# Kernel optimization log

Measured on AMD Instinct MI355X. Metric: run time of the kernel, lower is better.

## Reference

```python
import jax, jax.numpy as jnp
import numpy as np

B, T, C, H = 1, 4096, 768, 12
D = C // H  # 64


def setup_inputs() -> dict:
    key = jax.random.key(0)
    k1, k2, k3, k4, k5 = jax.random.split(key, 5)
    x = jax.random.normal(k1, (B, T, C), dtype=jnp.float32)
    # causal mask: 1.0 where attention is DISALLOWED (strict upper triangle)
    mask = (1.0 - jnp.tril(jnp.ones((T, T), dtype=jnp.float32)))[None, None, :, :]
    s_attn = 1.0 / np.sqrt(C)
    W_qkv = jax.random.normal(k2, (C, 3 * C), dtype=jnp.float32) * s_attn
    b_qkv = jnp.zeros((3 * C,), dtype=jnp.float32)
    W_proj = jax.random.normal(k3, (C, C), dtype=jnp.float32) * s_attn
    b_proj = jnp.zeros((C,), dtype=jnp.float32)
    return {"x": x, "mask": mask, "W_qkv": W_qkv, "b_qkv": b_qkv,
            "W_proj": W_proj, "b_proj": b_proj}


def reference(x, mask, W_qkv, b_qkv, W_proj, b_proj):
    qkv = jnp.einsum('btc,cf->btf', x, W_qkv) + b_qkv        # [B,T,3C]
    q, k, v = jnp.split(qkv, 3, axis=2)
    # [B,T,C] -> [B,H,T,D]
    q = q.reshape(B, T, H, D).transpose(0, 2, 1, 3)
    k = k.reshape(B, T, H, D).transpose(0, 2, 1, 3)
    v = v.reshape(B, T, H, D).transpose(0, 2, 1, 3)
    att = jnp.einsum('bhqd,bhkd->bhqk', q, k) * (1.0 / jnp.sqrt(jnp.float32(D)))
    att = att + mask * (-1e9)
    att = jax.nn.softmax(att, axis=-1)                        # [B,H,T,T]
    y = jnp.einsum('bhqk,bhkd->bhqd', att, v)                 # [B,H,T,D]
    y = y.transpose(0, 2, 1, 3).reshape(B, T, C)
    return jnp.einsum('btc,cf->btf', y, W_proj) + b_proj
```

## Files before the change

kernel.cpp:

```cpp
#include <hip/hip_runtime.h>

typedef unsigned short u16t;
typedef short bf16x8 __attribute__((ext_vector_type(8)));
typedef short bf16x4 __attribute__((ext_vector_type(4)));
typedef float f32x4 __attribute__((ext_vector_type(4)));

#define T_SEQ 4096
#define NH    12
#define HD    64
#define C3    2304
#define CDIM  768
#define STRIP_KV 512
#define SLOTS 144

__device__ __forceinline__ float bf2f(u16t u) {
  union { unsigned int i; float f; } c; c.i = ((unsigned int)u) << 16; return c.f;
}
__device__ __forceinline__ u16t f2bf(float f) {
  union { float f; unsigned int i; } c; c.f = f;
  unsigned int u = c.i;
  u += 0x7fffu + ((u >> 16) & 1u);
  return (u16t)(u >> 16);
}
__device__ __forceinline__ void gload16(const u16t* g, u16t* l) {
  __builtin_amdgcn_global_load_lds((const __attribute__((address_space(1))) void*)g,
                                   (__attribute__((address_space(3))) void*)l,
                                   16, 0, 0);
}

#define BARRIER_LGKM() __asm__ __volatile__("s_waitcnt lgkmcnt(0)\n\ts_barrier" ::: "memory")

__global__ __launch_bounds__(256) void convert_to_bf16(const float* __restrict__ in,
                                                       u16t* __restrict__ out, int n) {
  int i = blockIdx.x * 256 + threadIdx.x;
  const int stride = gridDim.x * 256;
  for (; i < n; i += stride) out[i] = f2bf(in[i]);
}

__global__ __launch_bounds__(256) void transpose_weights(const float* __restrict__ Wqkv,
                                                         const float* __restrict__ Wproj,
                                                         u16t* __restrict__ WqkvT,
                                                         u16t* __restrict__ WprojT) {
  __shared__ u16t tile[32][33];
  const int z = blockIdx.z;
  const int Cc = z ? CDIM : C3;
  if (z && blockIdx.x >= (unsigned)(CDIM / 32)) return;
  const float* in = z ? Wproj : Wqkv;
  u16t* out = z ? WprojT : WqkvT;
  const int tx = threadIdx.x, ty = threadIdx.y;
  const int c0 = blockIdx.x * 32, r0 = blockIdx.y * 32;
#pragma unroll
  for (int i = 0; i < 32; i += 8)
    tile[ty + i][tx] = f2bf(in[(size_t)(r0 + ty + i) * Cc + c0 + tx]);
  __syncthreads();
#pragma unroll
  for (int i = 0; i < 32; i += 8)
    out[(size_t)(c0 + ty + i) * CDIM + r0 + tx] = tile[tx][ty + i];
}

template <int MT, int NF, bool OUTF32>
__global__ __launch_bounds__(256) void gemm_bt_bias(
    const u16t* __restrict__ A, const u16t* __restrict__ Bt,
    const float* __restrict__ bias, void* __restrict__ Cout,
    int M, int N, int K) {
  constexpr int BN = 32 * NF;
  constexpr int MI = MT / 32;
  __shared__ u16t lA[MT * 32];
  __shared__ u16t lB[BN * 32];
  const int t = threadIdx.x;
  const int lane = t & 63;
  const int wid  = t >> 6;
  const int quad = lane >> 4, l16 = lane & 15;
  const int m0 = blockIdx.y * MT, n0 = blockIdx.x * BN;
  const int wm = (wid >> 1) * (16 * MI), wn = (wid & 1) * (16 * NF);

  f32x4 acc[MI][NF];
#pragma unroll
  for (int i = 0; i < MI; ++i)
#pragma unroll
    for (int j = 0; j < NF; ++j) acc[i][j] = (f32x4){0.f, 0.f, 0.f, 0.f};

  for (int k0 = 0; k0 < K; k0 += 32) {
    {
#pragma unroll
      for (int rd = 0; rd < MT / 64; ++rd) {
        const int e = rd * 256 + t;
        gload16(A + (size_t)(m0 + (e >> 2)) * K + k0 + (e & 3) * 8, &lA[e * 8]);
      }
#pragma unroll
      for (int rd = 0; rd < NF / 2; ++rd) {
        const int e = rd * 256 + t;
        gload16(Bt + (size_t)(n0 + (e >> 2)) * K + k0 + (e & 3) * 8, &lB[e * 8]);
      }
    }
    __syncthreads();
    bf16x8 af[MI], bfr[NF];
#pragma unroll
    for (int i = 0; i < MI; ++i)
      af[i] = *(const bf16x8*)&lA[(wm + i * 16 + l16) * 32 + quad * 8];
#pragma unroll
    for (int i = 0; i < NF; ++i)
      bfr[i] = *(const bf16x8*)&lB[(wn + i * 16 + l16) * 32 + quad * 8];
#pragma unroll
    for (int i = 0; i < MI; ++i)
#pragma unroll
      for (int j = 0; j < NF; ++j)
        acc[i][j] = __builtin_amdgcn_mfma_f32_16x16x32_bf16(af[i], bfr[j], acc[i][j], 0, 0, 0);
    __syncthreads();
  }

#pragma unroll
  for (int j = 0; j < NF; ++j) {
    const int col = n0 + wn + j * 16 + l16;
    const float bv = bias[col];
#pragma unroll
    for (int i = 0; i < MI; ++i) {
      const int rowb = m0 + wm + i * 16 + quad * 4;
#pragma unroll
      for (int r = 0; r < 4; ++r) {
        const float val = acc[i][j][r] + bv;
        const size_t idx = (size_t)(rowb + r) * N + col;
        if (OUTF32) ((float*)Cout)[idx] = val;
        else        ((u16t*)Cout)[idx] = f2bf(val);
      }
    }
  }
}

#define KSTR 88
#define VSTR 80

__global__ __launch_bounds__(256, 3) void attn_partial(const u16t* __restrict__ qkv,
                                                       u16t* __restrict__ pO,
                                                       float* __restrict__ pL) {
  const int h     = blockIdx.x;
  const int strip = blockIdx.y;
  const int qt    = 31 - (int)blockIdx.z;
  const int q0 = qt * 128;
  const int kv_begin = strip * STRIP_KV;
  const int kv_end   = q0 + 128;
  if (kv_begin >= kv_end) return;
  const int kv_stop = (kv_begin + STRIP_KV < kv_end) ? kv_begin + STRIP_KV : kv_end;
  const int a = qt >> 2, b = qt & 3;
  const int slot = (a + 1) * (2 * a + b) + strip;

  __shared__ u16t lK[64 * KSTR];
  __shared__ u16t lVt[64 * VSTR];

  const int t = threadIdx.x;
  const int lane = t & 63;
  const int wid  = t >> 6;
  const int quad = lane >> 4, l16 = lane & 15;
  const int wr = q0 + wid * 32;

  const int krow = t >> 3, kcol = (t & 7) * 8;
  const int vk0 = 4 * (t >> 4);
  const int vd0 = 4 * (t & 15);
  const int vswz = (t & 3) << 3;
  const u16t* Kbase = qkv + CDIM + h * HD;
  const u16t* Vbase = qkv + 2 * CDIM + h * HD;

  bf16x8 qf[2][2];
#pragma unroll
  for (int qn = 0; qn < 2; ++qn) {
    const int row = wr + qn * 16 + l16;
#pragma unroll
    for (int kd = 0; kd < 2; ++kd)
      qf[qn][kd] = *(const bf16x8*)(qkv + (size_t)row * C3 + h * HD + kd * 32 + quad * 8);
  }

  f32x4 oaccT[4][2];
  float lacc[2] = {0.f, 0.f};
#pragma unroll
  for (int dn = 0; dn < 4; ++dn)
#pragma unroll
    for (int qn = 0; qn < 2; ++qn) oaccT[dn][qn] = (f32x4){0.f, 0.f, 0.f, 0.f};

  const float SC = 0.125f * 1.4426950408889634f;
  const int pswz = ((l16 >> 2) & 3) << 3;

  uint4 kreg0, kreg1;
  union { uint2 u; u16t hw[4]; } vreg[4];

#define LOAD_TILE(KV0)                                                        \
  do {                                                                        \
    kreg0 = *(const uint4*)(Kbase + (size_t)((KV0) + krow) * C3 + kcol);      \
    kreg1 = *(const uint4*)(Kbase + (size_t)((KV0) + krow + 32) * C3 + kcol); \
    _Pragma("unroll")                                                         \
    for (int i = 0; i < 4; ++i)                                               \
      vreg[i].u = *(const uint2*)(Vbase + (size_t)((KV0) + vk0 + i) * C3 + vd0); \
  } while (0)

#define STORE_TILE()                                                          \
  do {                                                                        \
    *(uint4*)&lK[krow * KSTR + kcol] = kreg0;                                 \
    *(uint4*)&lK[(krow + 32) * KSTR + kcol] = kreg1;                          \
    _Pragma("unroll")                                                         \
    for (int j = 0; j < 4; ++j) {                                             \
      union { uint2 u; u16t hw[4]; } w;                                       \
      w.hw[0] = vreg[0].hw[j]; w.hw[1] = vreg[1].hw[j];                       \
      w.hw[2] = vreg[2].hw[j]; w.hw[3] = vreg[3].hw[j];                       \
      *(uint2*)&lVt[(vd0 + j) * VSTR + (vk0 ^ vswz)] = w.u;                   \
    }                                                                         \
  } while (0)

  LOAD_TILE(kv_begin);
  STORE_TILE();

  for (int kv0 = kv_begin; kv0 < kv_stop; kv0 += 64) {
    const bool havenext = (kv0 + 64 < kv_stop);
    if (havenext) LOAD_TILE(kv0 + 64);
    BARRIER_LGKM();

    if (kv0 <= wr + 31) {
      f32x4 sacc[4][2];
#pragma unroll
      for (int kvt = 0; kvt < 4; ++kvt) {
        bf16x8 kf0 = *(const bf16x8*)&lK[(kvt * 16 + l16) * KSTR + quad * 8];
        bf16x8 kf1 = *(const bf16x8*)&lK[(kvt * 16 + l16) * KSTR + 32 + quad * 8];
#pragma unroll
        for (int qn = 0; qn < 2; ++qn) {
          f32x4 s = (f32x4){0.f, 0.f, 0.f, 0.f};
          s = __builtin_amdgcn_mfma_f32_16x16x32_bf16(kf0, qf[qn][0], s, 0, 0, 0);
          s = __builtin_amdgcn_mfma_f32_16x16x32_bf16(kf1, qf[qn][1], s, 0, 0, 0);
          sacc[kvt][qn] = s;
        }
      }
      const bool need_mask = (kv0 + 63 > wr);
      bf16x4 pbf[4][2];
#pragma unroll
      for (int kvt = 0; kvt < 4; ++kvt)
#pragma unroll
        for (int qn = 0; qn < 2; ++qn) {
          const int qg = wr + qn * 16 + l16;
          bf16x4 pb;
#pragma unroll
          for (int r = 0; r < 4; ++r) {
            const int kvg = kv0 + kvt * 16 + quad * 4 + r;
            float pv = __builtin_amdgcn_exp2f(sacc[kvt][qn][r] * SC);
            if (need_mask && (kvg > qg)) pv = 0.f;
            lacc[qn] += pv;
            pb[r] = (short)f2bf(pv);
          }
          pbf[kvt][qn] = pb;
        }
#pragma unroll
      for (int kvt = 0; kvt < 4; ++kvt) {
        const int kvcol = (kvt * 16 + quad * 4) ^ pswz;
#pragma unroll
        for (int dn = 0; dn < 4; ++dn) {
          bf16x4 vf = *(const bf16x4*)&lVt[(dn * 16 + l16) * VSTR + kvcol];
#pragma unroll
          for (int qn = 0; qn < 2; ++qn)
            oaccT[dn][qn] = __builtin_amdgcn_mfma_f32_16x16x16bf16_1k(
                vf, pbf[kvt][qn], oaccT[dn][qn], 0, 0, 0);
        }
      }
    }
    BARRIER_LGKM();
    if (havenext) STORE_TILE();
  }

#pragma unroll
  for (int qn = 0; qn < 2; ++qn) {
    lacc[qn] += __shfl_xor(lacc[qn], 16);
    lacc[qn] += __shfl_xor(lacc[qn], 32);
  }
  {
    u16t* scr = &lVt[wid * 16 * 80];
    u16t* po = pO + ((size_t)h * SLOTS + slot) * 128 * HD;
    float* pl = pL + ((size_t)h * SLOTS + slot) * 128;
#pragma unroll
    for (int qn = 0; qn < 2; ++qn) {
#pragma unroll
      for (int dn = 0; dn < 4; ++dn) {
        bf16x4 w;
#pragma unroll
        for (int r = 0; r < 4; ++r) w[r] = (short)f2bf(oaccT[dn][qn][r]);
        *(bf16x4*)&scr[l16 * 80 + dn * 16 + quad * 4] = w;
      }
      __asm__ __volatile__("s_waitcnt lgkmcnt(0)" ::: "memory");
      const int ql = wid * 32 + qn * 16 + l16;
      uint4 w0 = *(const uint4*)&scr[l16 * 80 + quad * 16];
      uint4 w1 = *(const uint4*)&scr[l16 * 80 + quad * 16 + 8];
      u16t* dst = po + (size_t)ql * HD + quad * 16;
      *(uint4*)dst = w0;
      *(uint4*)(dst + 8) = w1;
      if (quad == 0) pl[ql] = lacc[qn];
      __asm__ __volatile__("s_waitcnt lgkmcnt(0)" ::: "memory");
    }
  }
#undef LOAD_TILE
#undef STORE_TILE
}

__global__ __launch_bounds__(256) void attn_normalize(const u16t* __restrict__ pO,
                                                      const float* __restrict__ pL,
                                                      u16t* __restrict__ y) {
  const int i = blockIdx.x * 256 + threadIdx.x;
  const int q = i / (CDIM / 4), c4 = (i % (CDIM / 4)) * 4;
  const int h = c4 >> 6, d = c4 & 63;
  const int qt = q >> 7, ql = q & 127;
  const int a = qt >> 2, b = qt & 3;
  const int base = (a + 1) * (2 * a + b);
  const int ns = a + 1;
  float o0 = 0.f, o1 = 0.f, o2 = 0.f, o3 = 0.f, l = 0.f;
  for (int s = 0; s < ns; ++s) {
    const size_t sl = (size_t)h * SLOTS + base + s;
    union { uint2 u; u16t hw[4]; } v;
    v.u = *(const uint2*)&pO[(sl * 128 + ql) * HD + d];
    o0 += bf2f(v.hw[0]); o1 += bf2f(v.hw[1]);
    o2 += bf2f(v.hw[2]); o3 += bf2f(v.hw[3]);
    l += pL[sl * 128 + ql];
  }
  const float rl = 1.0f / l;
  union { uint2 u; u16t hw[4]; } w;
  w.hw[0] = f2bf(o0 * rl); w.hw[1] = f2bf(o1 * rl);
  w.hw[2] = f2bf(o2 * rl); w.hw[3] = f2bf(o3 * rl);
  *(uint2*)&y[(size_t)q * CDIM + c4] = w.u;
}

extern "C" void kernel_launch(void* const* d_in, const int* in_sizes, int n_in,
                              void* d_out, int out_size, void* d_ws, size_t ws_size,
                              hipStream_t stream) {
  const float* x     = (const float*)d_in[0];
  const float* Wqkv  = (const float*)d_in[2];
  const float* bqkv  = (const float*)d_in[3];
  const float* Wproj = (const float*)d_in[4];
  const float* bproj = (const float*)d_in[5];

  u16t* qkv    = (u16t*)d_ws;
  u16t* ybuf   = qkv    + (size_t)T_SEQ * C3;
  u16t* WqkvT  = ybuf   + (size_t)T_SEQ * CDIM;
  u16t* WprojT = WqkvT  + (size_t)C3 * CDIM;
  u16t* pO     = WprojT + (size_t)CDIM * CDIM;
  float* pL    = (float*)(pO + (size_t)NH * SLOTS * 128 * HD);

  convert_to_bf16<<<1024, 256, 0, stream>>>(x, ybuf, T_SEQ * CDIM);
  transpose_weights<<<dim3(C3 / 32, CDIM / 32, 2), dim3(32, 8), 0, stream>>>(
      Wqkv, Wproj, WqkvT, WprojT);
  gemm_bt_bias<128, 4, false><<<dim3(C3 / 128, T_SEQ / 128), 256, 0, stream>>>(
      ybuf, WqkvT, bqkv, qkv, T_SEQ, C3, CDIM);
  attn_partial<<<dim3(NH, 8, T_SEQ / 128), 256, 0, stream>>>(qkv, pO, pL);
  attn_normalize<<<(T_SEQ * CDIM / 4) / 256, 256, 0, stream>>>(pO, pL, ybuf);
  gemm_bt_bias<64, 2, true><<<dim3(CDIM / 64, T_SEQ / 64), 256, 0, stream>>>(
      ybuf, WprojT, bproj, d_out, T_SEQ, CDIM, CDIM);
}
```

Baseline: 241.7 us.

## Fold softmax scale into QKV GEMM, compute row sums via MFMA, pack bf16 conversions

Moves the softmax scale times log2(e) into the QKV GEMM epilogue by scaling the Q columns, so the attention inner loop calls exp2 on raw scores. Row-sum accumulation is moved from per-element VALU adds plus cross-lane shuffles to an MFMA against a vector of ones on the bf16 probabilities. Float-to-bf16 conversion switches to packed two-at-a-time intrinsics, and the attention kernel raises its occupancy hint from 3 to 5 with a wider V stride. The changes cut VALU work in the softmax path, but the row sums now come from bf16-rounded probabilities, and the higher occupancy target may force register spills.

```diff
diff --git a/kernel.cpp b/kernel.cpp
--- a/kernel.cpp
+++ b/kernel.cpp
@@ -1,4 +1,5 @@
 #include <hip/hip_runtime.h>
+#include <hip/hip_bf16.h>
 
 typedef unsigned short u16t;
 typedef short bf16x8 __attribute__((ext_vector_type(8)));
@@ -12,6 +13,7 @@
 #define CDIM  768
 #define STRIP_KV 512
 #define SLOTS 144
+#define SC_F  0.18033688011112042f
 
 __device__ __forceinline__ float bf2f(u16t u) {
   union { unsigned int i; float f; } c; c.i = ((unsigned int)u) << 16; return c.f;
@@ -21,6 +23,10 @@
   unsigned int u = c.i;
   u += 0x7fffu + ((u >> 16) & 1u);
   return (u16t)(u >> 16);
+}
+__device__ __forceinline__ unsigned pk2bf(float a, float b) {
+  __hip_bfloat162 h = __float22bfloat162_rn(make_float2(a, b));
+  union { __hip_bfloat162 h; unsigned u; } c; c.h = h; return c.u;
 }
 __device__ __forceinline__ void gload16(const u16t* g, u16t* l) {
   __builtin_amdgcn_global_load_lds((const __attribute__((address_space(1))) void*)g,
@@ -62,7 +68,7 @@
 __global__ __launch_bounds__(256) void gemm_bt_bias(
     const u16t* __restrict__ A, const u16t* __restrict__ Bt,
     const float* __restrict__ bias, void* __restrict__ Cout,
-    int M, int N, int K) {
+    int M, int N, int K, int qcols, float qscale) {
   constexpr int BN = 32 * NF;
   constexpr int MI = MT / 32;
   __shared__ u16t lA[MT * 32];
@@ -113,12 +119,13 @@
   for (int j = 0; j < NF; ++j) {
     const int col = n0 + wn + j * 16 + l16;
     const float bv = bias[col];
+    const float cs = (col < qcols) ? qscale : 1.0f;
 #pragma unroll
     for (int i = 0; i < MI; ++i) {
       const int rowb = m0 + wm + i * 16 + quad * 4;
 #pragma unroll
       for (int r = 0; r < 4; ++r) {
-        const float val = acc[i][j][r] + bv;
+        const float val = (acc[i][j][r] + bv) * cs;
         const size_t idx = (size_t)(rowb + r) * N + col;
         if (OUTF32) ((float*)Cout)[idx] = val;
         else        ((u16t*)Cout)[idx] = f2bf(val);
@@ -128,9 +135,9 @@
 }
 
 #define KSTR 88
-#define VSTR 80
-
-__global__ __launch_bounds__(256, 3) void attn_partial(const u16t* __restrict__ qkv,
+#define VSTR 88
+
+__global__ __launch_bounds__(256, 5) void attn_partial(const u16t* __restrict__ qkv,
                                                        u16t* __restrict__ pO,
                                                        float* __restrict__ pL) {
   const int h     = blockIdx.x;
@@ -170,13 +177,17 @@
   }
 
   f32x4 oaccT[4][2];
-  float lacc[2] = {0.f, 0.f};
+  f32x4 laccT[2];
 #pragma unroll
   for (int dn = 0; dn < 4; ++dn)
 #pragma unroll
     for (int qn = 0; qn < 2; ++qn) oaccT[dn][qn] = (f32x4){0.f, 0.f, 0.f, 0.f};
-
-  const float SC = 0.125f * 1.4426950408889634f;
+#pragma unroll
+  for (int qn = 0; qn < 2; ++qn) laccT[qn] = (f32x4){0.f, 0.f, 0.f, 0.f};
+  bf16x4 ones4;
+#pragma unroll
+  for (int i = 0; i < 4; ++i) ones4[i] = (short)0x3F80;
+
   const int pswz = ((l16 >> 2) & 3) << 3;
 
   uint4 kreg0, kreg1;
@@ -233,20 +244,26 @@
 #pragma unroll
         for (int qn = 0; qn < 2; ++qn) {
           const int qg = wr + qn * 16 + l16;
-          bf16x4 pb;
+          float pv[4];
 #pragma unroll
           for (int r = 0; r < 4; ++r) {
             const int kvg = kv0 + kvt * 16 + quad * 4 + r;
-            float pv = __builtin_amdgcn_exp2f(sacc[kvt][qn][r] * SC);
-            if (need_mask && (kvg > qg)) pv = 0.f;
-            lacc[qn] += pv;
-            pb[r] = (short)f2bf(pv);
+            float p = __builtin_amdgcn_exp2f(sacc[kvt][qn][r]);
+            if (need_mask && (kvg > qg)) p = 0.f;
+            pv[r] = p;
           }
-          pbf[kvt][qn] = pb;
+          union { bf16x4 v; unsigned u[2]; } pw;
+          pw.u[0] = pk2bf(pv[0], pv[1]);
+          pw.u[1] = pk2bf(pv[2], pv[3]);
+          pbf[kvt][qn] = pw.v;
         }
 #pragma unroll
       for (int kvt = 0; kvt < 4; ++kvt) {
         const int kvcol = (kvt * 16 + quad * 4) ^ pswz;
+#pragma unroll
+        for (int qn = 0; qn < 2; ++qn)
+          laccT[qn] = __builtin_amdgcn_mfma_f32_16x16x16bf16_1k(
+              ones4, pbf[kvt][qn], laccT[qn], 0, 0, 0);
 #pragma unroll
         for (int dn = 0; dn < 4; ++dn) {
           bf16x4 vf = *(const bf16x4*)&lVt[(dn * 16 + l16) * VSTR + kvcol];
@@ -261,11 +278,6 @@
     if (havenext) STORE_TILE();
   }
 
-#pragma unroll
-  for (int qn = 0; qn < 2; ++qn) {
-    lacc[qn] += __shfl_xor(lacc[qn], 16);
-    lacc[qn] += __shfl_xor(lacc[qn], 32);
-  }
   {
     u16t* scr = &lVt[wid * 16 * 80];
     u16t* po = pO + ((size_t)h * SLOTS + slot) * 128 * HD;
@@ -274,10 +286,10 @@
     for (int qn = 0; qn < 2; ++qn) {
 #pragma unroll
       for (int dn = 0; dn < 4; ++dn) {
-        bf16x4 w;
-#pragma unroll
-        for (int r = 0; r < 4; ++r) w[r] = (short)f2bf(oaccT[dn][qn][r]);
-        *(bf16x4*)&scr[l16 * 80 + dn * 16 + quad * 4] = w;
+        union { bf16x4 v; unsigned u[2]; } w;
+        w.u[0] = pk2bf(oaccT[dn][qn][0], oaccT[dn][qn][1]);
+        w.u[1] = pk2bf(oaccT[dn][qn][2], oaccT[dn][qn][3]);
+        *(bf16x4*)&scr[l16 * 80 + dn * 16 + quad * 4] = w.v;
       }
       __asm__ __volatile__("s_waitcnt lgkmcnt(0)" ::: "memory");
       const int ql = wid * 32 + qn * 16 + l16;
@@ -286,7 +298,7 @@
       u16t* dst = po + (size_t)ql * HD + quad * 16;
       *(uint4*)dst = w0;
       *(uint4*)(dst + 8) = w1;
-      if (quad == 0) pl[ql] = lacc[qn];
+      if (quad == 0) pl[ql] = laccT[qn][0];
       __asm__ __volatile__("s_waitcnt lgkmcnt(0)" ::: "memory");
     }
   }
@@ -314,10 +326,10 @@
     l += pL[sl * 128 + ql];
   }
   const float rl = 1.0f / l;
-  union { uint2 u; u16t hw[4]; } w;
-  w.hw[0] = f2bf(o0 * rl); w.hw[1] = f2bf(o1 * rl);
-  w.hw[2] = f2bf(o2 * rl); w.hw[3] = f2bf(o3 * rl);
-  *(uint2*)&y[(size_t)q * CDIM + c4] = w.u;
+  union { uint2 u; unsigned w[2]; } wv;
+  wv.w[0] = pk2bf(o0 * rl, o1 * rl);
+  wv.w[1] = pk2bf(o2 * rl, o3 * rl);
+  *(uint2*)&y[(size_t)q * CDIM + c4] = wv.u;
 }
 
 extern "C" void kernel_launch(void* const* d_in, const int* in_sizes, int n_in,
@@ -340,9 +352,9 @@
   transpose_weights<<<dim3(C3 / 32, CDIM / 32, 2), dim3(32, 8), 0, stream>>>(
       Wqkv, Wproj, WqkvT, WprojT);
   gemm_bt_bias<128, 4, false><<<dim3(C3 / 128, T_SEQ / 128), 256, 0, stream>>>(
-      ybuf, WqkvT, bqkv, qkv, T_SEQ, C3, CDIM);
+      ybuf, WqkvT, bqkv, qkv, T_SEQ, C3, CDIM, CDIM, SC_F);
   attn_partial<<<dim3(NH, 8, T_SEQ / 128), 256, 0, stream>>>(qkv, pO, pL);
   attn_normalize<<<(T_SEQ * CDIM / 4) / 256, 256, 0, stream>>>(pO, pL, ybuf);
   gemm_bt_bias<64, 2, true><<<dim3(CDIM / 64, T_SEQ / 64), 256, 0, stream>>>(
-      ybuf, WprojT, bproj, d_out, T_SEQ, CDIM, CDIM);
-}
+      ybuf, WprojT, bproj, d_out, T_SEQ, CDIM, CDIM, 0, 1.0f);
+}
```

After: 344.5 us. 1.43x slower.
